# Performance work log

Measured on AMD Instinct MI355X. Metric: run time of the kernel, lower is better.

Reference implementation:

```python
import jax, jax.numpy as jnp
import numpy as np

K = 3       # kernel_size
STRIDE = 1
PAD = 1

def _unfold(x, k, s, p):
    # torch.nn.functional.unfold with dilation=1; returns [N, C*k*k, L]
    N, C, H, W = x.shape
    out_H = (H - k + 2 * p) // s + 1
    out_W = (W - k + 2 * p) // s + 1
    xp = jnp.pad(x, ((0, 0), (0, 0), (p, p), (p, p)))
    # k*k = 9 static slices; ordering (c, kh, kw) matches torch unfold
    patches = [xp[:, :, i:i + (out_H - 1) * s + 1:s, j:j + (out_W - 1) * s + 1:s]
               for i in range(k) for j in range(k)]
    patches = jnp.stack(patches, axis=2)              # [N, C, k*k, out_H, out_W]
    return patches.reshape(N, C * k * k, out_H * out_W), out_H, out_W


def setup_inputs() -> dict:
    key = jax.random.key(0)
    k1, k2 = jax.random.split(key)
    N, C, H, W = 2, 32, 64, 64
    out_ch = 32
    L = H * W  # stride=1, pad=1, k=3 -> same spatial size
    features = jax.random.normal(k1, (N, C, H, W), dtype=jnp.float32)
    filters = jax.random.normal(k2, (N, L, C * K * K, out_ch), dtype=jnp.float32) * 0.05
    return {"features": features, "filters": filters}


def reference(features, filters):
    unf, out_H, out_W = _unfold(features, K, STRIDE, PAD)   # [N, Ckk, L]
    feat = unf.transpose(0, 2, 1)                           # [N, L, Ckk]
    # per-location matvec: [N,L,1,Ckk] @ [N,L,Ckk,O] -> [N,L,O]
    res = jnp.einsum('nlk,nlko->nol', feat, filters)        # [N, O, L]
    N = features.shape[0]
    res = res.reshape(N, filters.shape[-1], out_H, out_W)
    return jax.nn.relu(res)
```

## Files before the change

### kernel.cpp

```cpp
#include <hip/hip_runtime.h>


#define C_     32
#define H_     64
#define W_     64
#define O_     32
#define CKK_   288
#define L_     (H_ * W_)

__global__ __launch_bounds__(256) void convfilt_kernel(
    const float* __restrict__ features,
    const float* __restrict__ filters,
    float* __restrict__ out)
{
    const int loc = blockIdx.x;
    const int n   = loc / L_;
    const int l   = loc % L_;
    const int oh  = l / W_;
    const int ow  = l % W_;
    const int t   = threadIdx.x;

    __shared__ float s_feat[CKK_];
    __shared__ float s_red[4][O_];

    for (int idx = t; idx < CKK_; idx += 256) {
        const int c  = idx / 9;
        const int r  = idx % 9;
        const int kh = r / 3;
        const int kw = r % 3;
        const int ih = oh + kh - 1;
        const int iw = ow + kw - 1;
        float v = 0.0f;
        if (ih >= 0 && ih < H_ && iw >= 0 && iw < W_)
            v = features[((n * C_ + c) * H_ + ih) * W_ + iw];
        s_feat[idx] = v;
    }
    __syncthreads();

    const float4* __restrict__ fptr =
        (const float4*)(filters + (size_t)loc * (CKK_ * O_));

    float acc0 = 0.f, acc1 = 0.f, acc2 = 0.f, acc3 = 0.f;
#pragma unroll
    for (int i = 0; i < 9; ++i) {
        const float4 f  = fptr[i * 256 + t];
        const float  fv = s_feat[(i * 256 + t) >> 3];
        acc0 = fmaf(f.x, fv, acc0);
        acc1 = fmaf(f.y, fv, acc1);
        acc2 = fmaf(f.z, fv, acc2);
        acc3 = fmaf(f.w, fv, acc3);
    }

#pragma unroll
    for (int s = 8; s < 64; s <<= 1) {
        acc0 += __shfl_down(acc0, s);
        acc1 += __shfl_down(acc1, s);
        acc2 += __shfl_down(acc2, s);
        acc3 += __shfl_down(acc3, s);
    }

    const int wave = t >> 6;
    const int lane = t & 63;
    if (lane < 8) {
        const int ob = lane * 4;
        s_red[wave][ob + 0] = acc0;
        s_red[wave][ob + 1] = acc1;
        s_red[wave][ob + 2] = acc2;
        s_red[wave][ob + 3] = acc3;
    }
    __syncthreads();

    if (t < O_) {
        float r = s_red[0][t] + s_red[1][t] + s_red[2][t] + s_red[3][t];
        r = fmaxf(r, 0.0f);
        out[((size_t)n * O_ + t) * L_ + l] = r;
    }
}

extern "C" void kernel_launch(void* const* d_in, const int* in_sizes, int n_in,
                              void* d_out, int out_size, void* d_ws, size_t ws_size,
                              hipStream_t stream)
{
    const float* features = (const float*)d_in[0];
    const float* filters  = (const float*)d_in[1];
    float* out            = (float*)d_out;

    const int N = in_sizes[0] / (C_ * H_ * W_);
    const int grid = N * L_;

    convfilt_kernel<<<grid, 256, 0, stream>>>(features, filters, out);
}
```

Before: 396.4 us.

## Map one spatial location per wavefront with nontemporal filter streaming

Each block now handles four locations, one per 64-lane wave, instead of one location per block. Each wave streams its own 36 KB filter slice with nontemporal float4 loads and reduces with shuffles only. This removes the cross-wave shared-memory reduction and one block barrier, and cuts the block count by four. The cost is a longer serial load loop per wave, fewer waves in flight per location, and scattered stride-L output stores.

```diff
diff --git a/kernel.cpp b/kernel.cpp
--- a/kernel.cpp
+++ b/kernel.cpp
@@ -1,79 +1,77 @@
 #include <hip/hip_runtime.h>
 
 
-#define C_     32
-#define H_     64
-#define W_     64
-#define O_     32
-#define CKK_   288
-#define L_     (H_ * W_)
+#define C_   32
+#define H_   64
+#define W_   64
+#define O_   32
+#define CKK_ 288
+#define L_   (H_ * W_)
+
+typedef float vf4 __attribute__((ext_vector_type(4)));
 
 __global__ __launch_bounds__(256) void convfilt_kernel(
     const float* __restrict__ features,
     const float* __restrict__ filters,
     float* __restrict__ out)
 {
-    const int loc = blockIdx.x;
-    const int n   = loc / L_;
-    const int l   = loc % L_;
-    const int oh  = l / W_;
-    const int ow  = l % W_;
-    const int t   = threadIdx.x;
+    const int wave = threadIdx.x >> 6;
+    const int lane = threadIdx.x & 63;
+    const int loc  = blockIdx.x * 4 + wave;
 
-    __shared__ float s_feat[CKK_];
-    __shared__ float s_red[4][O_];
+    const int n  = loc >> 12;
+    const int l  = loc & (L_ - 1);
+    const int oh = l >> 6;
+    const int ow = l & (W_ - 1);
 
-    for (int idx = t; idx < CKK_; idx += 256) {
-        const int c  = idx / 9;
-        const int r  = idx % 9;
-        const int kh = r / 3;
-        const int kw = r % 3;
-        const int ih = oh + kh - 1;
-        const int iw = ow + kw - 1;
-        float v = 0.0f;
-        if (ih >= 0 && ih < H_ && iw >= 0 && iw < W_)
-            v = features[((n * C_ + c) * H_ + ih) * W_ + iw];
-        s_feat[idx] = v;
+    __shared__ float sf[4][CKK_];
+    float* __restrict__ s = sf[wave];
+
+    #pragma unroll
+    for (int q = 0; q < 5; ++q) {
+        const int e = q * 64 + lane;
+        if (e < CKK_) {
+            const int c  = e / 9;
+            const int r  = e % 9;
+            const int ih = oh + (r / 3) - 1;
+            const int iw = ow + (r % 3) - 1;
+            float v = 0.0f;
+            if ((unsigned)ih < (unsigned)H_ && (unsigned)iw < (unsigned)W_)
+                v = features[((n * C_ + c) * H_ + ih) * W_ + iw];
+            s[e] = v;
+        }
     }
     __syncthreads();
 
-    const float4* __restrict__ fptr =
-        (const float4*)(filters + (size_t)loc * (CKK_ * O_));
+    const vf4* __restrict__ fp =
+        (const vf4*)(filters + (size_t)loc * (CKK_ * O_));
+    const int g = lane >> 3;
 
-    float acc0 = 0.f, acc1 = 0.f, acc2 = 0.f, acc3 = 0.f;
-#pragma unroll
-    for (int i = 0; i < 9; ++i) {
-        const float4 f  = fptr[i * 256 + t];
-        const float  fv = s_feat[(i * 256 + t) >> 3];
-        acc0 = fmaf(f.x, fv, acc0);
-        acc1 = fmaf(f.y, fv, acc1);
-        acc2 = fmaf(f.z, fv, acc2);
-        acc3 = fmaf(f.w, fv, acc3);
+    float a0 = 0.f, a1 = 0.f, a2 = 0.f, a3 = 0.f;
+    #pragma unroll
+    for (int j = 0; j < 36; ++j) {
+        const vf4  f  = __builtin_nontemporal_load(fp + j * 64 + lane);
+        const float fv = s[j * 8 + g];
+        a0 = fmaf(f.x, fv, a0);
+        a1 = fmaf(f.y, fv, a1);
+        a2 = fmaf(f.z, fv, a2);
+        a3 = fmaf(f.w, fv, a3);
     }
 
-#pragma unroll
-    for (int s = 8; s < 64; s <<= 1) {
-        acc0 += __shfl_down(acc0, s);
-        acc1 += __shfl_down(acc1, s);
-        acc2 += __shfl_down(acc2, s);
-        acc3 += __shfl_down(acc3, s);
+    #pragma unroll
+    for (int st = 8; st < 64; st <<= 1) {
+        a0 += __shfl_down(a0, st);
+        a1 += __shfl_down(a1, st);
+        a2 += __shfl_down(a2, st);
+        a3 += __shfl_down(a3, st);
     }
 
-    const int wave = t >> 6;
-    const int lane = t & 63;
     if (lane < 8) {
-        const int ob = lane * 4;
-        s_red[wave][ob + 0] = acc0;
-        s_red[wave][ob + 1] = acc1;
-        s_red[wave][ob + 2] = acc2;
-        s_red[wave][ob + 3] = acc3;
-    }
-    __syncthreads();
-
-    if (t < O_) {
-        float r = s_red[0][t] + s_red[1][t] + s_red[2][t] + s_red[3][t];
-        r = fmaxf(r, 0.0f);
-        out[((size_t)n * O_ + t) * L_ + l] = r;
+        float* op = out + ((size_t)n * O_ + lane * 4) * L_ + l;
+        op[0 * L_] = fmaxf(a0, 0.f);
+        op[1 * L_] = fmaxf(a1, 0.f);
+        op[2 * L_] = fmaxf(a2, 0.f);
+        op[3 * L_] = fmaxf(a3, 0.f);
     }
 }
 
@@ -85,8 +83,9 @@
     const float* filters  = (const float*)d_in[1];
     float* out            = (float*)d_out;
 
-    const int N = in_sizes[0] / (C_ * H_ * W_);
-    const int grid = N * L_;
+    const int N     = in_sizes[0] / (C_ * H_ * W_);
+    const int total = N * L_;
+    const int grid  = total / 4;
 
     convfilt_kernel<<<grid, 256, 0, stream>>>(features, filters, out);
 }
```

After: 375.2 us. -5.3%, faster.
